# Optimization experiments

Measured on AMD Instinct MI355X. Metric: run time of the kernel, lower is better.

The kernel has to match this reference:

```python
import jax, jax.numpy as jnp
import numpy as np

EPS = 1.0        # model eps for norm
STEP = 0.05      # step_size

def _norm(x):
    # torch: x / (eps + x.std(-1, keepdims=True)), torch std is unbiased (ddof=1)
    return x / (EPS + jnp.std(x, axis=-1, keepdims=True, ddof=1))

def setup_inputs() -> dict:
    key = jax.random.key(0)
    B, L, LM = 4, 512, 64
    G, E, K, D, KN = 32000, 256, 8, 6, 4
    ks = jax.random.split(key, 16)
    s = lambda k, shape, fan: (jax.random.normal(k, shape, jnp.float32) / np.sqrt(fan)).astype(jnp.float32)
    return dict(
        masked=jax.random.randint(ks[0], (B, L), 0, G),
        unmasked=jax.random.randint(ks[1], (B, L), 0, G),
        mask=jax.random.randint(ks[2], (B, LM), 0, L),
        embed=s(ks[3], (G, E), E),                 # embedding table
        Wt=s(ks[4], (D, E, E), E),                 # transition.weight per layer
        bt=jnp.zeros((D, E), jnp.float32),         # transition.bias per layer
        Wtc=s(ks[5], (D, E, E), E),                # transcore.weight per layer
        Wq=s(ks[6], (D, K * E, E), E),             # attq.weight per layer
        Wd=s(ks[7], (D, K * E, K * E), K * E),     # att_dense.weight per layer
        Wo=s(ks[8], (D, K * E, E), K * E),         # atto.weight per layer
        Wu=s(ks[9], (D, E, E), E),                 # updater.weight per layer
        Wem=s(ks[10], (E, E), E),                  # emittor.weight (head)
        Wkc=s(ks[11], (E * KN, E), E),             # kchoice.weight (head)
        bkc=jnp.zeros((E * KN,), jnp.float32),     # kchoice.bias (head)
    )

def reference(masked, unmasked, mask, embed, Wt, bt, Wtc, Wq, Wd, Wo, Wu, Wem, Wkc, bkc):
    B, L = masked.shape
    G, E = embed.shape
    K = Wq.shape[1] // E
    KN = Wkc.shape[0] // E
    inv_sqrt_e = 1.0 / np.sqrt(E)

    z = _norm(embed[masked])          # [B,L,E] input image
    xsa0 = z

    def step(xsa, p):
        wt, bt_, wtc, wq, wd, wo, wu = p
        # roll-based left/right transitions
        xsad = jax.nn.relu(jnp.roll(xsa, 1, axis=1) @ wt) @ wtc
        xsad = xsad + jax.nn.relu(jnp.roll(xsa, -1, axis=1) @ wtc.T) @ wt.T
        xsad = xsad + z @ wu.T + bt_   # use_input_image
        # QKV_Attention with kernel-expanded head dim: q [B,L,K,E] vs keys/values xsa [B,L,E]
        q = (xsa @ wq.T).reshape(B, L, K, E)
        h = jnp.einsum('blke,bme->blkm', q, xsa) * inv_sqrt_e
        pijk = jax.nn.softmax(h, axis=-1)
        y = jnp.einsum('blkm,bme->blke', pijk, xsa).reshape(B, L, K * E)
        # mode 1: Dense -> Relu -> Dense
        xid = jax.nn.relu(y @ wd.T) @ wo     # [B,L,E]
        xsad = _norm(xsad + xid)             # use_gradnorm
        xsa = _norm(xsa + STEP * xsad)       # use_layernorm
        return xsa, None

    xsa, _ = jax.lax.scan(step, xsa0, (Wt, bt, Wtc, Wq, Wd, Wo, Wu))

    # k-choice loss head (callback_cent)
    LM = mask.shape[1]
    lptok = jnp.take_along_axis(xsa, mask[:, :, None], axis=1)         # [B,LM,E]
    xx = (lptok @ Wkc.T + bkc).reshape(B, LM * KN, E)                  # kchoice
    xx = jnp.einsum('bnl,ble->bne', jnp.einsum('bne,ble->bnl', xx, xsa), xsa)
    logits = (xx @ Wem) @ embed.T                                      # [B,LM*KN,G]
    k_lp = jax.nn.log_softmax(logits, axis=-1).reshape(B, LM, KN, G)
    lptok = jax.scipy.special.logsumexp(k_lp, axis=2) - jnp.log(jnp.float32(KN))
    tgt = jnp.take_along_axis(unmasked, mask, axis=1)                  # [B,LM]
    cent = jnp.take_along_axis(lptok, tgt[:, :, None], axis=-1)[:, :, 0]
    return -cent.mean(-1)                                              # [B]
```

## Files before the change

### kernel.cpp

```cpp
#include <hip/hip_runtime.h>
#include <hip/hip_bf16.h>
#include <math.h>

typedef __bf16 bf16x8 __attribute__((ext_vector_type(8)));
typedef float floatx4 __attribute__((ext_vector_type(4)));

__device__ __forceinline__ short f2b(float f) {
  __hip_bfloat16 h = __float2bfloat16(f);
  return *reinterpret_cast<short*>(&h);
}
__device__ __forceinline__ float b2f(short s) {
  unsigned u = ((unsigned)(unsigned short)s) << 16;
  float f;
  __builtin_memcpy(&f, &u, 4);
  return f;
}

__device__ __forceinline__ void gl2lds16(const void* g, void* l) {
  __builtin_amdgcn_global_load_lds((__attribute__((address_space(1))) const void*)g,
                                   (__attribute__((address_space(3))) void*)l, 16, 0, 0);
}

__device__ __forceinline__ float block_sum(float v, float* sdata) {
#pragma unroll
  for (int o = 32; o > 0; o >>= 1) v += __shfl_down(v, o, 64);
  __syncthreads();
  int lane = threadIdx.x & 63, wid = threadIdx.x >> 6;
  if (lane == 0) sdata[wid] = v;
  __syncthreads();
  float s = 0.f;
  int nw = blockDim.x >> 6;
  for (int i = 0; i < nw; i++) s += sdata[i];
  return s;
}

__global__ void cvt_kernel(const float* __restrict__ src, short* __restrict__ dst, long n4) {
  long i = (long)blockIdx.x * blockDim.x + threadIdx.x;
  if (i < n4) {
    float4 v = ((const float4*)src)[i];
    short4 o;
    o.x = f2b(v.x); o.y = f2b(v.y); o.z = f2b(v.z); o.w = f2b(v.w);
    ((short4*)dst)[i] = o;
  }
}

__global__ void cvt2_kernel(const float* __restrict__ src, short* __restrict__ dst,
                            int ldS, int ldD, long sS, long sD) {
  src += (size_t)blockIdx.z * sS;
  dst += (size_t)blockIdx.z * sD;
  int c = blockIdx.x * 32 + threadIdx.x;
  int r0 = blockIdx.y * 32 + threadIdx.y;
#pragma unroll
  for (int i = 0; i < 32; i += 8)
    dst[(size_t)(r0 + i) * ldD + c] = f2b(src[(size_t)(r0 + i) * ldS + c]);
}

__global__ void cvtT2_kernel(const float* __restrict__ src, short* __restrict__ dst,
                             int ldS, int ldD, long sS, long sD) {
  src += (size_t)blockIdx.z * sS;
  dst += (size_t)blockIdx.z * sD;
  __shared__ float tile[32][33];
  int r0 = blockIdx.y * 32, c0 = blockIdx.x * 32;
  int tx = threadIdx.x, ty = threadIdx.y;
#pragma unroll
  for (int i = 0; i < 32; i += 8)
    tile[ty + i][tx] = src[(size_t)(r0 + ty + i) * ldS + c0 + tx];
  __syncthreads();
#pragma unroll
  for (int i = 0; i < 32; i += 8)
    dst[(size_t)(c0 + ty + i) * ldD + r0 + tx] = f2b(tile[tx][ty + i]);
}

__global__ void embed_norm_kernel(const int* __restrict__ masked,
                                  const float* __restrict__ embed,
                                  float* __restrict__ xsa, short* __restrict__ xsa_bf,
                                  short* __restrict__ xsaT_bf, short* __restrict__ catA,
                                  int E, int L, int ldA, int zoff) {
  int row = blockIdx.x;
  int g = masked[row];
  __shared__ float sdata[8];
  float x = embed[(size_t)g * E + threadIdx.x];
  float mean = block_sum(x, sdata) / E;
  float d = x - mean;
  float var = block_sum(d * d, sdata) / (E - 1);
  float val = x / (1.0f + sqrtf(var));
  size_t off = (size_t)row * E + threadIdx.x;
  xsa[off] = val;
  short b = f2b(val);
  xsa_bf[off] = b;
  catA[(size_t)row * ldA + zoff + threadIdx.x] = b;
  int bb = row / L, l = row - bb * L;
  xsaT_bf[((size_t)bb * E + threadIdx.x) * L + l] = b;
}

template <int BM, int BN, int OUT_BF16, int ASUM>
__global__ __launch_bounds__(256) void bgemm_kernel(
    const short* __restrict__ A, int lda, long sA,
    const short* __restrict__ B, int ldb, long sB,
    void* __restrict__ Cv, int ldc, long sC,
    short* __restrict__ C2b, int ldc2, int ncut,
    int Ksz, float alpha, const float* __restrict__ bias,
    int relu, int expo, int shiftA, int shiftB, int ns1, int ns2, int Lroll,
    int ksplit, long ksC) {
  constexpr int WM = BM / 2, WN = BN / 2;
  constexpr int MT = WM / 16, NT = WN / 16;
  constexpr int NCH = (BM + BN) * 8;
  constexpr int LPT = NCH / 256;
  int bz = blockIdx.z, kz = 0;
  if (ksplit > 1) {
    bz = blockIdx.z / ksplit;
    kz = blockIdx.z - bz * ksplit;
  }
  int Kper = Ksz / ksplit;
  int koff = kz * Kper;
  A += (size_t)bz * sA + koff;
  B += (size_t)bz * sB + koff;
  float* Cf = (float*)Cv + (size_t)bz * sC + (size_t)kz * ksC;
  short* Cb = (short*)Cv + (size_t)bz * sC;
  int m0 = blockIdx.y * BM, n0 = blockIdx.x * BN;
  int shift = (n0 < ns1) ? shiftA : ((n0 < ns2) ? shiftB : 0);
  int zone2 = (C2b != nullptr) && (n0 >= ncut);
  __shared__ short S[2][(BM + BN) * 64];
  int tid = threadIdx.x, lane = tid & 63, w = tid >> 6;
  int wm = (w & 1) * WM, wn = (w >> 1) * WN;
  int ml = lane & 15, q4 = lane >> 4, sw = ml & 7;

  const short* src[LPT];
#pragma unroll
  for (int i = 0; i < LPT; i++) {
    int q = i * 256 + w * 64 + lane;
    if (q < BM * 8) {
      int m = q >> 3, cl = q & 7, cs = cl ^ (m & 7);
      int mg = m0 + m;
      if (shift != 0) {
        int bb = mg / Lroll, l = mg - bb * Lroll;
        l = (l + shift + Lroll) % Lroll;
        mg = bb * Lroll + l;
      }
      src[i] = A + (size_t)mg * lda + cs * 8;
    } else {
      int qb = q - BM * 8;
      int n = qb >> 3, cl = qb & 7, cs = cl ^ (n & 7);
      src[i] = B + (size_t)(n0 + n) * ldb + cs * 8;
    }
  }
#pragma unroll
  for (int i = 0; i < LPT; i++)
    gl2lds16(src[i], &S[0][(i * 256 + w * 64) * 8]);
  floatx4 acc[MT][NT] = {};
  floatx4 sumacc[ASUM ? MT : 1] = {};
  bf16x8 ones;
#pragma unroll
  for (int i = 0; i < 8; i++) ones[i] = (__bf16)1.0f;
  int nT = Kper >> 6;
  for (int t = 0; t < nT; t++) {
    __syncthreads();
    int cur = t & 1;
    if (t + 1 < nT) {
      int nxt = cur ^ 1, ko = (t + 1) * 64;
#pragma unroll
      for (int i = 0; i < LPT; i++)
        gl2lds16(src[i] + ko, &S[nxt][(i * 256 + w * 64) * 8]);
    }
#pragma unroll
    for (int kk = 0; kk < 2; kk++) {
      int j = kk * 4 + q4;
      bf16x8 af[MT], bg[NT];
#pragma unroll
      for (int mt = 0; mt < MT; mt++) {
        int r = wm + mt * 16 + ml;
        af[mt] = *reinterpret_cast<const bf16x8*>(&S[cur][r * 64 + (j ^ sw) * 8]);
      }
#pragma unroll
      for (int nt = 0; nt < NT; nt++) {
        int r = wn + nt * 16 + ml;
        bg[nt] = *reinterpret_cast<const bf16x8*>(&S[cur][BM * 64 + r * 64 + (j ^ sw) * 8]);
      }
#pragma unroll
      for (int mt = 0; mt < MT; mt++)
#pragma unroll
        for (int nt = 0; nt < NT; nt++)
          acc[mt][nt] = __builtin_amdgcn_mfma_f32_16x16x32_bf16(af[mt], bg[nt], acc[mt][nt], 0, 0, 0);
      if (ASUM)
#pragma unroll
        for (int mt = 0; mt < MT; mt++)
          sumacc[mt] = __builtin_amdgcn_mfma_f32_16x16x32_bf16(af[mt], ones, sumacc[mt], 0, 0, 0);
    }
  }
#pragma unroll
  for (int mt = 0; mt < MT; mt++) {
    float sinv[4];
    if (ASUM) {
#pragma unroll
      for (int r = 0; r < 4; r++) sinv[r] = 1.f / sumacc[mt][r];
    }
#pragma unroll
    for (int nt = 0; nt < NT; nt++) {
      floatx4 v = acc[mt][nt];
#pragma unroll
      for (int r = 0; r < 4; r++) {
        int grow = m0 + wm + mt * 16 + q4 * 4 + r;
        int gcol = n0 + wn + nt * 16 + ml;
        float x = alpha * v[r];
        if (ASUM) x *= sinv[r];
        if (bias && kz == 0) x += bias[gcol];
        if (relu && !zone2) x = fmaxf(x, 0.f);
        if (expo) x = exp2f(x);
        if (OUT_BF16) {
          if (zone2)
            C2b[(size_t)grow * ldc2 + (gcol - ncut)] = f2b(x);
          else
            Cb[(size_t)grow * ldc + gcol] = f2b(x);
        } else {
          Cf[(size_t)grow * ldc + gcol] = x;
        }
      }
    }
  }
}

__global__ void addnorm_kernel(const float* __restrict__ xA, const float* __restrict__ xB,
                               float* __restrict__ xsa, short* __restrict__ xsa_bf,
                               short* __restrict__ xsaT_bf, int E, int L) {
  int row = blockIdx.x, t = threadIdx.x;
  __shared__ float sdata[8];
  size_t off = (size_t)row * E + t;
  float s1 = xA[off] + xB[off];
  float mean = block_sum(s1, sdata) / E;
  float d = s1 - mean;
  float var = block_sum(d * d, sdata) / (E - 1);
  float n1 = s1 / (1.f + sqrtf(var));
  float t2 = xsa[off] + 0.05f * n1;
  float mean2 = block_sum(t2, sdata) / E;
  float d2 = t2 - mean2;
  float var2 = block_sum(d2 * d2, sdata) / (E - 1);
  float res = t2 / (1.f + sqrtf(var2));
  xsa[off] = res;
  short b = f2b(res);
  xsa_bf[off] = b;
  int bb = row / L, l = row - bb * L;
  xsaT_bf[((size_t)bb * E + t) * L + l] = b;
}

__global__ void gather_kernel(const float* __restrict__ xsa, const int* __restrict__ mask,
                              const int* __restrict__ unmasked,
                              short* __restrict__ lptok_bf, int* __restrict__ tgt,
                              int L, int LM, int E) {
  int bi = blockIdx.x;
  int b = bi / LM;
  int pos = mask[bi];
  float v = xsa[((size_t)b * L + pos) * E + threadIdx.x];
  lptok_bf[(size_t)bi * E + threadIdx.x] = f2b(v);
  if (threadIdx.x == 0) tgt[bi] = unmasked[b * L + pos];
}

__global__ __launch_bounds__(256) void head_stats_kernel(
    const short* __restrict__ V, const short* __restrict__ Eb,
    float* __restrict__ stM, float* __restrict__ stS, int Ksz, int nch, int Mrows) {
  int t0 = blockIdx.x;
  int xcd = t0 & 7, j = t0 >> 3;
  int c = ((j >> 4) << 3) | xcd;
  if (c >= nch) return;
  int m0 = (j & 15) * 64, n0 = c * 128;
  __shared__ short S[2][(64 + 128) * 64];
  int tid = threadIdx.x, lane = tid & 63, w = tid >> 6;
  int wm = (w & 1) * 32, wn = (w >> 1) * 64;
  int ml = lane & 15, q4 = lane >> 4, sw = ml & 7;
  const short* src[6];
#pragma unroll
  for (int i = 0; i < 6; i++) {
    int q = i * 256 + w * 64 + lane;
    if (q < 512) {
      int m = q >> 3, cl = q & 7, cs = cl ^ (m & 7);
      src[i] = V + (size_t)(m0 + m) * Ksz + cs * 8;
    } else {
      int qb = q - 512;
      int n = qb >> 3, cl = qb & 7, cs = cl ^ (n & 7);
      src[i] = Eb + (size_t)(n0 + n) * Ksz + cs * 8;
    }
  }
#pragma unroll
  for (int i = 0; i < 6; i++)
    gl2lds16(src[i], &S[0][(i * 256 + w * 64) * 8]);
  floatx4 acc[2][4] = {};
  int nT = Ksz >> 6;
  for (int t = 0; t < nT; t++) {
    __syncthreads();
    int cur = t & 1;
    if (t + 1 < nT) {
      int nxt = cur ^ 1, ko = (t + 1) * 64;
#pragma unroll
      for (int i = 0; i < 6; i++)
        gl2lds16(src[i] + ko, &S[nxt][(i * 256 + w * 64) * 8]);
    }
#pragma unroll
    for (int kk = 0; kk < 2; kk++) {
      int jj = kk * 4 + q4;
      bf16x8 af[2], bg[4];
#pragma unroll
      for (int mt = 0; mt < 2; mt++) {
        int r = wm + mt * 16 + ml;
        af[mt] = *reinterpret_cast<const bf16x8*>(&S[cur][r * 64 + (jj ^ sw) * 8]);
      }
#pragma unroll
      for (int nt = 0; nt < 4; nt++) {
        int r = wn + nt * 16 + ml;
        bg[nt] = *reinterpret_cast<const bf16x8*>(&S[cur][512 * 8 + r * 64 + (jj ^ sw) * 8]);
      }
#pragma unroll
      for (int mt = 0; mt < 2; mt++)
#pragma unroll
        for (int nt = 0; nt < 4; nt++)
          acc[mt][nt] = __builtin_amdgcn_mfma_f32_16x16x32_bf16(af[mt], bg[nt], acc[mt][nt], 0, 0, 0);
    }
  }
  __syncthreads();
  const float log2e = 1.4426950408889634f;
  float (*sred)[2] = (float (*)[2]) & S[0][0];
  float (*sred2)[2] = (float (*)[2]) & S[1][0];
  float mx[2][4];
#pragma unroll
  for (int mt = 0; mt < 2; mt++)
#pragma unroll
    for (int r = 0; r < 4; r++)
      mx[mt][r] = fmaxf(fmaxf(acc[mt][0][r], acc[mt][1][r]), fmaxf(acc[mt][2][r], acc[mt][3][r]));
#pragma unroll
  for (int off = 1; off < 16; off <<= 1)
#pragma unroll
    for (int mt = 0; mt < 2; mt++)
#pragma unroll
      for (int r = 0; r < 4; r++) mx[mt][r] = fmaxf(mx[mt][r], __shfl_xor(mx[mt][r], off, 64));
  if (ml == 0)
#pragma unroll
    for (int mt = 0; mt < 2; mt++)
#pragma unroll
      for (int r = 0; r < 4; r++) sred[wm + mt * 16 + q4 * 4 + r][w >> 1] = mx[mt][r];
  __syncthreads();
  float sm[2][4];
#pragma unroll
  for (int mt = 0; mt < 2; mt++)
#pragma unroll
    for (int r = 0; r < 4; r++) {
      int row = wm + mt * 16 + q4 * 4 + r;
      float fm = fmaxf(sred[row][0], sred[row][1]);
      float s = 0.f;
#pragma unroll
      for (int nt = 0; nt < 4; nt++) s += exp2f((acc[mt][nt][r] - fm) * log2e);
      sm[mt][r] = s;
    }
#pragma unroll
  for (int off = 1; off < 16; off <<= 1)
#pragma unroll
    for (int mt = 0; mt < 2; mt++)
#pragma unroll
      for (int r = 0; r < 4; r++) sm[mt][r] += __shfl_xor(sm[mt][r], off, 64);
  if (ml == 0)
#pragma unroll
    for (int mt = 0; mt < 2; mt++)
#pragma unroll
      for (int r = 0; r < 4; r++) sred2[wm + mt * 16 + q4 * 4 + r][w >> 1] = sm[mt][r];
  __syncthreads();
  if (tid < 64) {
    float fm = fmaxf(sred[tid][0], sred[tid][1]);
    stM[(size_t)c * Mrows + m0 + tid] = fm;
    stS[(size_t)c * Mrows + m0 + tid] = sred2[tid][0] + sred2[tid][1];
  }
}

__global__ void lse_reduce_kernel(const float* __restrict__ statsM,
                                  const float* __restrict__ statsS,
                                  float* __restrict__ lse, int nch, int Mrows) {
  int row = blockIdx.x, t = threadIdx.x;
  float m = -INFINITY, s = 0.f;
  for (int c = t; c < nch; c += blockDim.x) {
    float cm = statsM[(size_t)c * Mrows + row];
    float cs = statsS[(size_t)c * Mrows + row];
    float M = fmaxf(m, cm);
    s = s * expf(m - M) + cs * expf(cm - M);
    m = M;
  }
  __shared__ float sm[256], ss[256];
  sm[t] = m;
  ss[t] = s;
  __syncthreads();
  for (int o = 128; o > 0; o >>= 1) {
    if (t < o) {
      float m2 = sm[t + o], s2 = ss[t + o];
      float M = fmaxf(sm[t], m2);
      float sc = ss[t] * expf(sm[t] - M) + s2 * expf(m2 - M);
      sm[t] = M;
      ss[t] = sc;
    }
    __syncthreads();
  }
  if (t == 0) lse[row] = sm[0] + logf(ss[0]);
}

__global__ void logit_tgt_kernel(const short* __restrict__ V, const short* __restrict__ Eb,
                                 const int* __restrict__ tgt, float* __restrict__ lt,
                                 int E, int Nn, int KN, int LM) {
  int row = blockIdx.x;
  int b = row / Nn;
  int i = (row - b * Nn) / KN;
  int g = tgt[b * LM + i];
  __shared__ float sdata[8];
  float v = b2f(V[(size_t)row * E + threadIdx.x]) * b2f(Eb[(size_t)g * E + threadIdx.x]);
  float s = block_sum(v, sdata);
  if (threadIdx.x == 0) lt[row] = s;
}

__global__ void final_kernel(const float* __restrict__ lt, const float* __restrict__ lse,
                             float* __restrict__ out, int LM, int KN) {
  int b = blockIdx.x, i = threadIdx.x;
  int base = (b * LM + i) * KN;
  float m = -INFINITY;
  for (int k = 0; k < KN; k++) m = fmaxf(m, lt[base + k] - lse[base + k]);
  float s = 0.f;
  for (int k = 0; k < KN; k++) s += expf(lt[base + k] - lse[base + k] - m);
  float cent = m + logf(s) - logf((float)KN);
#pragma unroll
  for (int o = 32; o > 0; o >>= 1) cent += __shfl_down(cent, o, 64);
  if (i == 0) out[b] = -cent / LM;
}

static inline void bgemm(hipStream_t st, int cfg, const short* A, int lda, long sA,
                         const short* B, int ldb, long sB,
                         void* C, int ldc, long sC, int M, int N, int Ksz, int nb,
                         float alpha, const float* bias, int relu, int out_bf16,
                         int shiftA, int shiftB, int ns1, int ns2, int Lroll,
                         int expo = 0, int asum = 0,
                         short* C2 = nullptr, int ldc2 = 0, int ncut = 0,
                         int ksplit = 1, long ksC = 0) {
  dim3 block(256);
  int nz = nb * ksplit;
#define BG_ARGS A, lda, sA, B, ldb, sB, C, ldc, sC, C2, ldc2, ncut, Ksz, alpha, bias, relu, expo, shiftA, shiftB, ns1, ns2, Lroll, ksplit, ksC
  if (cfg == 0) {
    dim3 grid(N / 128, M / 128, nz);
    if (out_bf16)
      bgemm_kernel<128, 128, 1, 0><<<grid, block, 0, st>>>(BG_ARGS);
    else
      bgemm_kernel<128, 128, 0, 0><<<grid, block, 0, st>>>(BG_ARGS);
  } else if (cfg == 1) {
    dim3 grid(N / 64, M / 128, nz);
    if (out_bf16) {
      if (asum)
        bgemm_kernel<128, 64, 1, 1><<<grid, block, 0, st>>>(BG_ARGS);
      else
        bgemm_kernel<128, 64, 1, 0><<<grid, block, 0, st>>>(BG_ARGS);
    } else {
      bgemm_kernel<128, 64, 0, 0><<<grid, block, 0, st>>>(BG_ARGS);
    }
  } else {
    dim3 grid(N / 64, M / 64, nz);
    if (out_bf16)
      bgemm_kernel<64, 64, 1, 0><<<grid, block, 0, st>>>(BG_ARGS);
    else
      bgemm_kernel<64, 64, 0, 0><<<grid, block, 0, st>>>(BG_ARGS);
  }
#undef BG_ARGS
}

static inline void cvt(hipStream_t st, const float* src, short* dst, long n) {
  long n4 = n / 4;
  cvt_kernel<<<(int)((n4 + 255) / 256), 256, 0, st>>>(src, dst, n4);
}

static inline void cvt2(hipStream_t st, const float* src, short* dst, int R, int C,
                        int ldS, int ldD, long sS, long sD, int nb) {
  dim3 grid(C / 32, R / 32, nb), block(32, 8);
  cvt2_kernel<<<grid, block, 0, st>>>(src, dst, ldS, ldD, sS, sD);
}

static inline void cvtT2(hipStream_t st, const float* src, short* dst, int R, int C,
                         int ldS, int ldD, long sS, long sD, int nb) {
  dim3 grid(C / 32, R / 32, nb), block(32, 8);
  cvtT2_kernel<<<grid, block, 0, st>>>(src, dst, ldS, ldD, sS, sD);
}

extern "C" void kernel_launch(void* const* d_in, const int* in_sizes, int n_in,
                              void* d_out, int out_size, void* d_ws, size_t ws_size,
                              hipStream_t stream) {
  const int* masked = (const int*)d_in[0];
  const int* unmasked = (const int*)d_in[1];
  const int* mask = (const int*)d_in[2];
  const float* embed = (const float*)d_in[3];
  const float* Wt = (const float*)d_in[4];
  const float* bt = (const float*)d_in[5];
  const float* Wtc = (const float*)d_in[6];
  const float* Wq = (const float*)d_in[7];
  const float* Wd = (const float*)d_in[8];
  const float* Wo = (const float*)d_in[9];
  const float* Wu = (const float*)d_in[10];
  const float* Wem = (const float*)d_in[11];
  const float* Wkc = (const float*)d_in[12];
  const float* bkc = (const float*)d_in[13];

  const int B = out_size;
  const int BL = in_sizes[0];
  const int L = BL / B;
  const int BLM = in_sizes[2];
  const int LM = BLM / B;
  const int E = in_sizes[4] / in_sizes[5];
  const int D = in_sizes[5] / E;
  const int G = in_sizes[3] / E;
  const int K = in_sizes[7] / (D * E * E);
  const int KN = in_sizes[12] / (E * E);
  const int KE = K * E;
  const int N = LM * KN;
  const float inv_sqrt_e = 1.0f / sqrtf((float)E);
  const int nch = G / 128;
  const int E3 = 3 * E;
  const int KA = E3 + KE;
  const int NQ = 2 * E + KE;

  char* base = (char*)d_ws;
  size_t off = 0;
  auto carve = [&](size_t bytes) {
    char* p = base + off;
    off += (bytes + 255) & ~(size_t)255;
    return p;
  };
  float* xsa = (float*)carve((size_t)BL * E * 4);
  float* xsad = (float*)carve((size_t)2 * BL * E * 4);
  float* stM = (float*)carve((size_t)B * N * nch * 4);
  float* stS = (float*)carve((size_t)B * N * nch * 4);
  float* lse = (float*)carve((size_t)B * N * 4);
  float* lt = (float*)carve((size_t)B * N * 4);
  int* tgt = (int*)carve((size_t)B * LM * 4);
  short* xsa_bf = (short*)carve((size_t)BL * E * 2);
  short* xsaT_bf = (short*)carve((size_t)B * E * L * 2);
  short* catA = (short*)carve((size_t)BL * KA * 2);
  short* qy_bf = (short*)carve((size_t)BL * KE * 2);
  short* hP_bf = (short*)carve((size_t)B * L * K * L * 2);
  short* wd_all = (short*)carve((size_t)D * KE * KE * 2);
  short* BcatQ = (short*)carve((size_t)D * NQ * E * 2);
  short* Bcat2x = (short*)carve((size_t)D * E * KA * 2);
  short* embed_bf = (short*)carve((size_t)G * E * 2);
  short* WemT_bf = (short*)carve((size_t)E * E * 2);
  short* Wkc_bf = (short*)carve((size_t)KN * E * E * 2);
  short* gram_bf = (short*)carve((size_t)B * E * E * 2);
  short* xx_bf = (short*)carve((size_t)B * N * E * 2);
  short* xx2_bf = (short*)carve((size_t)B * N * E * 2);
  short* vv_bf = (short*)carve((size_t)B * N * E * 2);
  short* lptok_bf = (short*)carve((size_t)BLM * E * 2);

  cvt(stream, embed, embed_bf, (long)G * E);
  cvt(stream, Wd, wd_all, (long)D * KE * KE);
  cvt(stream, Wkc, Wkc_bf, (long)KN * E * E);
  cvtT2(stream, Wem, WemT_bf, E, E, E, E, 0, 0, 1);
  cvtT2(stream, Wt, BcatQ, E, E, E, E, (long)E * E, (long)NQ * E, D);
  cvt2(stream, Wtc, BcatQ + (size_t)E * E, E, E, E, E, (long)E * E, (long)NQ * E, D);
  cvt2(stream, Wq, BcatQ + (size_t)2 * E * E, KE, E, E, E, (long)KE * E, (long)NQ * E, D);
  cvtT2(stream, Wtc, Bcat2x, E, E, E, KA, (long)E * E, (long)E * KA, D);
  cvt2(stream, Wt, Bcat2x + E, E, E, E, KA, (long)E * E, (long)E * KA, D);
  cvt2(stream, Wu, Bcat2x + 2 * E, E, E, E, KA, (long)E * E, (long)E * KA, D);
  cvtT2(stream, Wo, Bcat2x + E3, KE, E, E, KA, (long)KE * E, (long)E * KA, D);

  embed_norm_kernel<<<BL, E, 0, stream>>>(masked, embed, xsa, xsa_bf, xsaT_bf, catA,
                                          E, L, KA, 2 * E);

  const float log2e = 1.4426950408889634f;
  for (int d = 0; d < D; d++) {
    const float* btl = bt + (size_t)d * E;
    bgemm(stream, 1, xsa_bf, E, 0, BcatQ + (size_t)d * NQ * E, E, 0,
          catA, KA, 0, BL, NQ, E, 1, 1.f, nullptr, 1, 1,
          -1, +1, E, 2 * E, L, 0, 0, qy_bf, KE, 2 * E);
    bgemm(stream, 0, qy_bf, E, (long)L * KE, xsa_bf, E, (long)L * E,
          hP_bf, L, (long)L * K * L, L * K, L, E, B, inv_sqrt_e * log2e, nullptr, 0, 1,
          0, 0, 0, 0, L, 1);
    bgemm(stream, 1, hP_bf, L, (long)L * K * L, xsaT_bf, L, (long)E * L,
          qy_bf, E, (long)L * KE, L * K, E, L, B, 1.f, nullptr, 0, 1,
          0, 0, 0, 0, L, 0, 1);
    bgemm(stream, 0, qy_bf, KE, 0, wd_all + (size_t)d * KE * KE, KE, 0,
          catA + E3, KA, 0, BL, KE, KE, 1, 1.f, nullptr, 1, 1, 0, 0, 0, 0, L);
    bgemm(stream, 2, catA, KA, 0, Bcat2x + (size_t)d * E * KA, KA, 0,
          xsad, E, 0, BL, E, KA, 1, 1.f, btl, 0, 0, 0, 0, 0, 0, L,
          0, 0, nullptr, 0, 0, 2, (long)BL * E);
    addnorm_kernel<<<BL, E, 0, stream>>>(xsad, xsad + (size_t)BL * E,
                                         xsa, xsa_bf, xsaT_bf, E, L);
  }

  gather_kernel<<<BLM, E, 0, stream>>>(xsa, mask, unmasked, lptok_bf, tgt, L, LM, E);
  bgemm(stream, 2, xsaT_bf, L, (long)E * L, xsaT_bf, L, (long)E * L,
        gram_bf, E, (long)E * E, E, E, L, B, 1.f, nullptr, 0, 1, 0, 0, 0, 0, L);
  bgemm(stream, 2, lptok_bf, E, 0, Wkc_bf, E, 0, xx_bf, KN * E, 0, BLM, KN * E, E, 1,
        1.f, bkc, 0, 1, 0, 0, 0, 0, L);
  bgemm(stream, 2, xx_bf, E, (long)N * E, gram_bf, E, (long)E * E,
        xx2_bf, E, (long)N * E, N, E, E, B, 1.f, nullptr, 0, 1, 0, 0, 0, 0, L);
  bgemm(stream, 2, xx2_bf, E, 0, WemT_bf, E, 0, vv_bf, E, 0, B * N, E, E, 1,
        1.f, nullptr, 0, 1, 0, 0, 0, 0, L);
  {
    int nchPad = (nch + 7) & ~7;
    head_stats_kernel<<<nchPad * 16, 256, 0, stream>>>(vv_bf, embed_bf, stM, stS,
                                                       E, nch, B * N);
  }
  lse_reduce_kernel<<<B * N, 256, 0, stream>>>(stM, stS, lse, nch, B * N);
  logit_tgt_kernel<<<B * N, E, 0, stream>>>(vv_bf, embed_bf, tgt, lt, E, N, KN, LM);
  final_kernel<<<B, LM, 0, stream>>>(lt, lse, (float*)d_out, LM, KN);
}
```

Before: 889.7 us.

## Keep head A-tile in registers, single-pass norms, fuse lse and target-logit kernels

The head stats kernel now loads each wave's 64-row V slice straight into registers for the whole K=256 and streams only the embedding tile through LDS, which shrinks shared memory and LDS traffic. The K loop is hard-coded to 4 steps, so it assumes E=256. Both norm kernels compute sum and sum of squares in one fused block reduction instead of two passes, which is less numerically robust. The lse reduction and the target-logit dot product are merged into a single launch.

```diff
diff --git a/kernel.cpp b/kernel.cpp
--- a/kernel.cpp
+++ b/kernel.cpp
@@ -32,6 +32,22 @@
   int nw = blockDim.x >> 6;
   for (int i = 0; i < nw; i++) s += sdata[i];
   return s;
+}
+
+__device__ __forceinline__ float2 block_sum2(float a, float b, float* sdata) {
+#pragma unroll
+  for (int o = 32; o > 0; o >>= 1) {
+    a += __shfl_down(a, o, 64);
+    b += __shfl_down(b, o, 64);
+  }
+  __syncthreads();
+  int lane = threadIdx.x & 63, wid = threadIdx.x >> 6;
+  if (lane == 0) { sdata[wid] = a; sdata[8 + wid] = b; }
+  __syncthreads();
+  float sa = 0.f, sb = 0.f;
+  int nw = blockDim.x >> 6;
+  for (int i = 0; i < nw; i++) { sa += sdata[i]; sb += sdata[8 + i]; }
+  return make_float2(sa, sb);
 }
 
 __global__ void cvt_kernel(const float* __restrict__ src, short* __restrict__ dst, long n4) {
@@ -78,11 +94,11 @@
                                   int E, int L, int ldA, int zoff) {
   int row = blockIdx.x;
   int g = masked[row];
-  __shared__ float sdata[8];
+  __shared__ float sdata[16];
   float x = embed[(size_t)g * E + threadIdx.x];
-  float mean = block_sum(x, sdata) / E;
-  float d = x - mean;
-  float var = block_sum(d * d, sdata) / (E - 1);
+  float2 ss = block_sum2(x, x * x, sdata);
+  float mean = ss.x / E;
+  float var = fmaxf((ss.y - E * mean * mean) / (E - 1), 0.f);
   float val = x / (1.0f + sqrtf(var));
   size_t off = (size_t)row * E + threadIdx.x;
   xsa[off] = val;
@@ -223,17 +239,17 @@
                                float* __restrict__ xsa, short* __restrict__ xsa_bf,
                                short* __restrict__ xsaT_bf, int E, int L) {
   int row = blockIdx.x, t = threadIdx.x;
-  __shared__ float sdata[8];
+  __shared__ float sdata[16];
   size_t off = (size_t)row * E + t;
   float s1 = xA[off] + xB[off];
-  float mean = block_sum(s1, sdata) / E;
-  float d = s1 - mean;
-  float var = block_sum(d * d, sdata) / (E - 1);
+  float2 r1 = block_sum2(s1, s1 * s1, sdata);
+  float mean = r1.x / E;
+  float var = fmaxf((r1.y - E * mean * mean) / (E - 1), 0.f);
   float n1 = s1 / (1.f + sqrtf(var));
   float t2 = xsa[off] + 0.05f * n1;
-  float mean2 = block_sum(t2, sdata) / E;
-  float d2 = t2 - mean2;
-  float var2 = block_sum(d2 * d2, sdata) / (E - 1);
+  float2 r2 = block_sum2(t2, t2 * t2, sdata);
+  float mean2 = r2.x / E;
+  float var2 = fmaxf((r2.y - E * mean2 * mean2) / (E - 1), 0.f);
   float res = t2 / (1.f + sqrtf(var2));
   xsa[off] = res;
   short b = f2b(res);
@@ -262,56 +278,57 @@
   int c = ((j >> 4) << 3) | xcd;
   if (c >= nch) return;
   int m0 = (j & 15) * 64, n0 = c * 128;
-  __shared__ short S[2][(64 + 128) * 64];
+  __shared__ short S[2][128 * 64];
   int tid = threadIdx.x, lane = tid & 63, w = tid >> 6;
   int wm = (w & 1) * 32, wn = (w >> 1) * 64;
   int ml = lane & 15, q4 = lane >> 4, sw = ml & 7;
-  const short* src[6];
-#pragma unroll
-  for (int i = 0; i < 6; i++) {
+
+  bf16x8 af[4][2][2];
+#pragma unroll
+  for (int mt = 0; mt < 2; mt++) {
+    const short* vp = V + (size_t)(m0 + wm + mt * 16 + ml) * Ksz + q4 * 8;
+#pragma unroll
+    for (int kt = 0; kt < 4; kt++)
+#pragma unroll
+      for (int kk = 0; kk < 2; kk++)
+        af[kt][kk][mt] = *reinterpret_cast<const bf16x8*>(vp + kt * 64 + kk * 32);
+  }
+
+  const short* src[4];
+#pragma unroll
+  for (int i = 0; i < 4; i++) {
     int q = i * 256 + w * 64 + lane;
-    if (q < 512) {
-      int m = q >> 3, cl = q & 7, cs = cl ^ (m & 7);
-      src[i] = V + (size_t)(m0 + m) * Ksz + cs * 8;
-    } else {
-      int qb = q - 512;
-      int n = qb >> 3, cl = qb & 7, cs = cl ^ (n & 7);
-      src[i] = Eb + (size_t)(n0 + n) * Ksz + cs * 8;
-    }
-  }
-#pragma unroll
-  for (int i = 0; i < 6; i++)
+    int n = q >> 3, cl = q & 7, cs = cl ^ (n & 7);
+    src[i] = Eb + (size_t)(n0 + n) * Ksz + cs * 8;
+  }
+#pragma unroll
+  for (int i = 0; i < 4; i++)
     gl2lds16(src[i], &S[0][(i * 256 + w * 64) * 8]);
   floatx4 acc[2][4] = {};
-  int nT = Ksz >> 6;
-  for (int t = 0; t < nT; t++) {
+#pragma unroll
+  for (int t = 0; t < 4; t++) {
     __syncthreads();
     int cur = t & 1;
-    if (t + 1 < nT) {
+    if (t + 1 < 4) {
       int nxt = cur ^ 1, ko = (t + 1) * 64;
 #pragma unroll
-      for (int i = 0; i < 6; i++)
+      for (int i = 0; i < 4; i++)
         gl2lds16(src[i] + ko, &S[nxt][(i * 256 + w * 64) * 8]);
     }
 #pragma unroll
     for (int kk = 0; kk < 2; kk++) {
       int jj = kk * 4 + q4;
-      bf16x8 af[2], bg[4];
-#pragma unroll
-      for (int mt = 0; mt < 2; mt++) {
-        int r = wm + mt * 16 + ml;
-        af[mt] = *reinterpret_cast<const bf16x8*>(&S[cur][r * 64 + (jj ^ sw) * 8]);
-      }
+      bf16x8 bg[4];
 #pragma unroll
       for (int nt = 0; nt < 4; nt++) {
         int r = wn + nt * 16 + ml;
-        bg[nt] = *reinterpret_cast<const bf16x8*>(&S[cur][512 * 8 + r * 64 + (jj ^ sw) * 8]);
+        bg[nt] = *reinterpret_cast<const bf16x8*>(&S[cur][r * 64 + (jj ^ sw) * 8]);
       }
 #pragma unroll
       for (int mt = 0; mt < 2; mt++)
 #pragma unroll
         for (int nt = 0; nt < 4; nt++)
-          acc[mt][nt] = __builtin_amdgcn_mfma_f32_16x16x32_bf16(af[mt], bg[nt], acc[mt][nt], 0, 0, 0);
+          acc[mt][nt] = __builtin_amdgcn_mfma_f32_16x16x32_bf16(af[t][kk][mt], bg[nt], acc[mt][nt], 0, 0, 0);
     }
   }
   __syncthreads();
@@ -367,10 +384,17 @@
   }
 }
 
-__global__ void lse_reduce_kernel(const float* __restrict__ statsM,
-                                  const float* __restrict__ statsS,
-                                  float* __restrict__ lse, int nch, int Mrows) {
+__global__ void lse_logit_kernel(const float* __restrict__ statsM,
+                                 const float* __restrict__ statsS,
+                                 const short* __restrict__ V, const short* __restrict__ Eb,
+                                 const int* __restrict__ tgt,
+                                 float* __restrict__ lse, float* __restrict__ lt,
+                                 int nch, int Mrows, int E, int Nn, int KN, int LM) {
   int row = blockIdx.x, t = threadIdx.x;
+  int b = row / Nn;
+  int i = (row - b * Nn) / KN;
+  int g = tgt[b * LM + i];
+  float v = b2f(V[(size_t)row * E + t]) * b2f(Eb[(size_t)g * E + t]);
   float m = -INFINITY, s = 0.f;
   for (int c = t; c < nch; c += blockDim.x) {
     float cm = statsM[(size_t)c * Mrows + row];
@@ -379,7 +403,9 @@
     s = s * expf(m - M) + cs * expf(cm - M);
     m = M;
   }
-  __shared__ float sm[256], ss[256];
+  __shared__ float sm[256], ss[256], sd[8];
+  float dot = block_sum(v, sd);
+  if (t == 0) lt[row] = dot;
   sm[t] = m;
   ss[t] = s;
   __syncthreads();
@@ -394,19 +420,6 @@
     __syncthreads();
   }
   if (t == 0) lse[row] = sm[0] + logf(ss[0]);
-}
-
-__global__ void logit_tgt_kernel(const short* __restrict__ V, const short* __restrict__ Eb,
-                                 const int* __restrict__ tgt, float* __restrict__ lt,
-                                 int E, int Nn, int KN, int LM) {
-  int row = blockIdx.x;
-  int b = row / Nn;
-  int i = (row - b * Nn) / KN;
-  int g = tgt[b * LM + i];
-  __shared__ float sdata[8];
-  float v = b2f(V[(size_t)row * E + threadIdx.x]) * b2f(Eb[(size_t)g * E + threadIdx.x]);
-  float s = block_sum(v, sdata);
-  if (threadIdx.x == 0) lt[row] = s;
 }
 
 __global__ void final_kernel(const float* __restrict__ lt, const float* __restrict__ lse,
@@ -594,7 +607,7 @@
     head_stats_kernel<<<nchPad * 16, 256, 0, stream>>>(vv_bf, embed_bf, stM, stS,
                                                        E, nch, B * N);
   }
-  lse_reduce_kernel<<<B * N, 256, 0, stream>>>(stM, stS, lse, nch, B * N);
-  logit_tgt_kernel<<<B * N, E, 0, stream>>>(vv_bf, embed_bf, tgt, lt, E, N, KN, LM);
+  lse_logit_kernel<<<B * N, 256, 0, stream>>>(stM, stS, vv_bf, embed_bf, tgt,
+                                              lse, lt, nch, B * N, E, N, KN, LM);
   final_kernel<<<B, LM, 0, stream>>>(lt, lse, (float*)d_out, LM, KN);
 }
```

New measurement: 880.5 us. About the same (-1.0%).
